# Performance work log

Hardware: AMD Instinct MI355X
Metric: run time of the kernel (lower is better)

Reference implementation:

```python
import jax, jax.numpy as jnp
import numpy as np

N = 100000   # nodes
F = 128      # input features
H = 128      # hidden = 2*output_dim
Z = 64       # output_dim
E = 1600000  # message-passing edges
EP = 200000  # pos/neg decode edges each


def setup_inputs() -> dict:
    key = jax.random.key(0)
    ks = jax.random.split(key, 6)
    x = jax.random.normal(ks[0], (N, F), dtype=jnp.float32)
    edge_index = jax.random.randint(ks[1], (2, E), 0, N, dtype=jnp.int64)
    pos_edge = jax.random.randint(ks[2], (2, EP), 0, N, dtype=jnp.int64)
    neg_edge = jax.random.randint(ks[3], (2, EP), 0, N, dtype=jnp.int64)
    W1 = jax.random.normal(ks[4], (F, H), dtype=jnp.float32) / np.float32(np.sqrt(F))
    b1 = jnp.zeros((H,), jnp.float32)
    W2 = jax.random.normal(ks[5], (H, Z), dtype=jnp.float32) / np.float32(np.sqrt(H))
    b2 = jnp.zeros((Z,), jnp.float32)
    return dict(x=x, W1=W1, b1=b1, W2=W2, b2=b2,
                edge_index=edge_index, pos_edge=pos_edge, neg_edge=neg_edge)


def _gcn_conv(x, src, dst, norm, W, b, n):
    # x' = scatter_add_dst(norm * (x @ W)[src]) + b   (GCNConv, sym-normalized, self-loops)
    h = x @ W                         # [N, out]
    msg = h[src] * norm[:, None]      # [E+N, out] gather + scale
    out = jax.ops.segment_sum(msg, dst, num_segments=n)
    return out + b


def reference(x, W1, b1, W2, b2, edge_index, pos_edge, neg_edge):
    # add self-loops (GCNConv default)
    loop = jnp.arange(N, dtype=edge_index.dtype)
    src = jnp.concatenate([edge_index[0], loop])
    dst = jnp.concatenate([edge_index[1], loop])
    # symmetric normalization deg^-1/2[src] * deg^-1/2[dst]
    deg = jax.ops.segment_sum(jnp.ones(dst.shape, x.dtype), dst, num_segments=N)
    dinv = jnp.where(deg > 0, jax.lax.rsqrt(deg), 0.0)
    norm = dinv[src] * dinv[dst]
    # encoder: GCN -> ReLU -> GCN
    h = jax.nn.relu(_gcn_conv(x, src, dst, norm, W1, b1, N))
    latent = _gcn_conv(h, src, dst, norm, W2, b2, N)
    # decoder: edge dot products on pos+neg edges
    e = jnp.concatenate([pos_edge, neg_edge], axis=-1)  # [2, 2*EP]
    logits = jnp.sum(latent[e[0]] * latent[e[1]], axis=-1)
    return logits
```

## Files before the change

### kernel.cpp

```cpp
#include <hip/hip_runtime.h>

#define N_NODES 100000
#define F_IN    128
#define H_DIM   128
#define Z_DIM   64
#define E_EDGES 1600000
#define EP_EDGES 200000

#define BSHIFT 7
#define NBUCK  ((N_NODES + 127) >> 7)
#define CHUNK  4096
#define NCHUNK ((E_EDGES + CHUNK - 1) / CHUNK)

typedef __attribute__((ext_vector_type(8))) short short8;
typedef __attribute__((ext_vector_type(4))) float f32x4;
typedef unsigned int uint;
typedef unsigned short ushort;

__device__ __forceinline__ ushort f2bf(float f) {
    uint u = __float_as_uint(f);
    u += 0x7fffu + ((u >> 16) & 1u);
    return (ushort)(u >> 16);
}
__device__ __forceinline__ float bflo(uint u) { return __uint_as_float(u << 16); }
__device__ __forceinline__ float bfhi(uint u) { return __uint_as_float(u & 0xffff0000u); }


__global__ __launch_bounds__(256) void wprep_kernel(const float* __restrict__ W1,
                                                    const float* __restrict__ W2,
                                                    ushort* __restrict__ W1T,
                                                    ushort* __restrict__ W2T,
                                                    int* __restrict__ gcur) {
    int i = blockIdx.x * 256 + threadIdx.x;
    if (i < 1024) gcur[i] = 0;
    if (i < 128 * 128) {
        int n = i >> 7, k = i & 127;
        W1T[i] = f2bf(W1[k * 128 + n]);
    }
    int j = i - 128 * 128;
    if (j >= 0 && j < 64 * 128) {
        int n = j >> 7, k = j & 127;
        W2T[j] = f2bf(W2[k * 64 + n]);
    }
}


__global__ __launch_bounds__(256) void bhist_kernel(const int* __restrict__ dst,
                                                    int* __restrict__ gcur,
                                                    int* __restrict__ tbl) {
    __shared__ int lh[NBUCK];
    for (int i = threadIdx.x; i < NBUCK; i += 256) lh[i] = 0;
    __syncthreads();
    int base = blockIdx.x * CHUNK;
    int end = min(base + CHUNK, E_EDGES);
    for (int e = base + threadIdx.x; e < end; e += 256)
        atomicAdd(&lh[dst[e] >> BSHIFT], 1);
    __syncthreads();
    int* trow = tbl + (size_t)blockIdx.x * NBUCK;
    for (int i = threadIdx.x; i < NBUCK; i += 256) {
        int c = lh[i];
        trow[i] = c;
        if (c) atomicAdd(&gcur[i], c);
    }
}


__global__ __launch_bounds__(1024) void bscan_kernel(int* __restrict__ gc) {
    __shared__ int s[1024];
    int t = threadIdx.x;
    int v = (t < NBUCK) ? gc[t] : 0;
    s[t] = v;
    __syncthreads();
    #pragma unroll
    for (int off = 1; off < 1024; off <<= 1) {
        int x = (t >= off) ? s[t - off] : 0;
        __syncthreads();
        s[t] += x;
        __syncthreads();
    }
    if (t < NBUCK) gc[t] = s[t] - v;
}


__global__ __launch_bounds__(512) void chunk_scan_kernel(int* __restrict__ tbl,
                                                         const int* __restrict__ gcur) {
    __shared__ int s[512];
    int b = blockIdx.x, t = threadIdx.x;
    int v = (t < NCHUNK) ? tbl[(size_t)t * NBUCK + b] : 0;
    s[t] = v;
    __syncthreads();
    #pragma unroll
    for (int off = 1; off < 512; off <<= 1) {
        int x = (t >= off) ? s[t - off] : 0;
        __syncthreads();
        s[t] += x;
        __syncthreads();
    }
    if (t < NCHUNK)
        tbl[(size_t)t * NBUCK + b] = gcur[b] + (s[t] - v);
}


__global__ __launch_bounds__(256) void bscatter_kernel(const int* __restrict__ src,
                                                       const int* __restrict__ dst,
                                                       const int* __restrict__ tbl,
                                                       int* __restrict__ sorted) {
    __shared__ int lbase[NBUCK];
    int c = blockIdx.x;
    const int* trow = tbl + (size_t)c * NBUCK;
    for (int i = threadIdx.x; i < NBUCK; i += 256) lbase[i] = trow[i];
    __syncthreads();
    int base = c * CHUNK;
    int end = min(base + CHUNK, E_EDGES);
    for (int e = base + threadIdx.x; e < end; e += 256) {
        int d = dst[e];
        int p = atomicAdd(&lbase[d >> BSHIFT], 1);
        sorted[p] = (src[e] << 7) | (d & 127);
    }
}


__global__ __launch_bounds__(256) void bucket_csr_kernel(const int* __restrict__ sorted,
                                                         const int* __restrict__ gcur,
                                                         int* __restrict__ csr,
                                                         int* __restrict__ ends,
                                                         float* __restrict__ dinv) {
    __shared__ int lcnt[4][128], lcur[4][128];
    int b = blockIdx.x, t = threadIdx.x;
    int wave = t >> 6;
    int bstart = gcur[b];
    int bend = (b + 1 < NBUCK) ? gcur[b + 1] : E_EDGES;
    if (t < 128) { lcnt[0][t] = 0; lcnt[1][t] = 0; }
    else { int u = t - 128; lcnt[2][u] = 0; lcnt[3][u] = 0; }
    __syncthreads();
    for (int i = bstart + t; i < bend; i += 256)
        atomicAdd(&lcnt[wave][sorted[i] & 127], 1);
    __syncthreads();
    if (t < 64) {
        int w0a = lcnt[0][t], w1a = lcnt[1][t], w2a = lcnt[2][t], w3a = lcnt[3][t];
        int w0b = lcnt[0][t + 64], w1b = lcnt[1][t + 64], w2b = lcnt[2][t + 64], w3b = lcnt[3][t + 64];
        int c0 = w0a + w1a + w2a + w3a;
        int c1 = w0b + w1b + w2b + w3b;
        int s0 = c0;
        #pragma unroll
        for (int d = 1; d < 64; d <<= 1) {
            int x = __shfl_up(s0, d, 64);
            if (t >= d) s0 += x;
        }
        int tot0 = __shfl(s0, 63, 64);
        int s1 = c1;
        #pragma unroll
        for (int d = 1; d < 64; d <<= 1) {
            int x = __shfl_up(s1, d, 64);
            if (t >= d) s1 += x;
        }
        s1 += tot0;
        int basea = bstart + s0 - c0;
        int baseb = bstart + s1 - c1;
        lcur[0][t] = basea;
        lcur[1][t] = basea + w0a;
        lcur[2][t] = basea + w0a + w1a;
        lcur[3][t] = basea + w0a + w1a + w2a;
        lcur[0][t + 64] = baseb;
        lcur[1][t + 64] = baseb + w0b;
        lcur[2][t + 64] = baseb + w0b + w1b;
        lcur[3][t + 64] = baseb + w0b + w1b + w2b;
        int n0 = b * 128 + t, n1 = n0 + 64;
        if (n0 < N_NODES) { ends[n0] = bstart + s0; dinv[n0] = rsqrtf(1.0f + (float)c0); }
        if (n1 < N_NODES) { ends[n1] = bstart + s1; dinv[n1] = rsqrtf(1.0f + (float)c1); }
    }
    __syncthreads();
    for (int i = bstart + t; i < bend; i += 256) {
        int v = sorted[i];
        int p = atomicAdd(&lcur[wave][v & 127], 1);
        csr[p] = v >> 7;
    }
}


template<int NC, bool A_F32>
__global__ __launch_bounds__(256) void gemm_mfma_kernel(const void* __restrict__ Ap,
                                                        const ushort* __restrict__ BT,
                                                        const float* __restrict__ dinv,
                                                        ushort* __restrict__ C, int M) {
    constexpr int NT = NC / 16;
    __shared__ ushort Bs[4 * NT * 64 * 8];

    for (int idx = threadIdx.x; idx < 4 * NT * 64; idx += 256) {
        int l   = idx & 63;
        int nt  = (idx >> 6) % NT;
        int kc  = idx / (64 * NT);
        int m16 = l & 15, quad = l >> 4;
        ((short8*)Bs)[idx] =
            *(const short8*)(BT + ((nt * 16 + m16) * 128 + kc * 32 + quad * 8));
    }
    __syncthreads();

    int wave = threadIdx.x >> 6, lane = threadIdx.x & 63;
    int m16 = lane & 15, quad = lane >> 4;
    int row0 = (blockIdx.x * 4 + wave) * 16;
    if (row0 >= M) return;
    int arow = row0 + m16;
    if (arow >= M) arow = M - 1;

    f32x4 acc[NT];
    #pragma unroll
    for (int t = 0; t < NT; ++t) acc[t] = (f32x4){0.f, 0.f, 0.f, 0.f};

    #pragma unroll
    for (int kc = 0; kc < 4; ++kc) {
        short8 a;
        if (A_F32) {
            const float* A = (const float*)Ap;
            const float4* p = (const float4*)(A + (size_t)arow * 128 + kc * 32 + quad * 8);
            float4 x0 = p[0], x1 = p[1];
            a[0] = (short)f2bf(x0.x); a[1] = (short)f2bf(x0.y);
            a[2] = (short)f2bf(x0.z); a[3] = (short)f2bf(x0.w);
            a[4] = (short)f2bf(x1.x); a[5] = (short)f2bf(x1.y);
            a[6] = (short)f2bf(x1.z); a[7] = (short)f2bf(x1.w);
        } else {
            a = *(const short8*)((const ushort*)Ap + (size_t)arow * 128 + kc * 32 + quad * 8);
        }
        #pragma unroll
        for (int nt = 0; nt < NT; ++nt) {
            short8 b = ((const short8*)Bs)[(kc * NT + nt) * 64 + lane];
            acc[nt] = __builtin_amdgcn_mfma_f32_16x16x32_bf16(a, b, acc[nt], 0, 0, 0);
        }
    }

    #pragma unroll
    for (int r = 0; r < 4; ++r) {
        int row = row0 + quad * 4 + r;
        if (row < M) {
            float dr = dinv[row];
            #pragma unroll
            for (int nt = 0; nt < NT; ++nt)
                C[(size_t)row * NC + nt * 16 + m16] = f2bf(acc[nt][r] * dr);
        }
    }
}


__global__ __launch_bounds__(256, 8) void gather128_kernel(const ushort* __restrict__ feat,
                                                           const float* __restrict__ bias,
                                                           const float* __restrict__ dinv,
                                                           const int* __restrict__ ends,
                                                           const int* __restrict__ csr,
                                                           ushort* __restrict__ out) {
    int wave = threadIdx.x >> 6, lane = threadIdx.x & 63;
    int q = lane >> 4, ql = lane & 15;
    int n = blockIdx.x * 4 + wave;
    const uint4* F = (const uint4*)feat;

    float a0 = 0.f, a1 = 0.f, a2 = 0.f, a3 = 0.f;
    float a4 = 0.f, a5 = 0.f, a6 = 0.f, a7 = 0.f;
    if (q == 0) {
        uint4 s = F[(uint)n * 16u + (uint)ql];
        a0 = bflo(s.x); a1 = bfhi(s.x); a2 = bflo(s.y); a3 = bfhi(s.y);
        a4 = bflo(s.z); a5 = bfhi(s.z); a6 = bflo(s.w); a7 = bfhi(s.w);
    }
    int j0 = n ? ends[n - 1] : 0, j1 = ends[n];
    for (int base = j0; base < j1; base += 64) {
        int m = min(64, j1 - base);
        int idxv = csr[base + min(lane, m - 1)];
        int nch = m >> 4;
        for (int c = 0; c < nch; ++c) {
            int e = c * 16 + q;
            int s0 = __shfl(idxv, e, 64);
            int s1 = __shfl(idxv, e + 4, 64);
            int s2 = __shfl(idxv, e + 8, 64);
            int s3 = __shfl(idxv, e + 12, 64);
            uint4 r0 = F[(uint)s0 * 16u + (uint)ql];
            uint4 r1 = F[(uint)s1 * 16u + (uint)ql];
            uint4 r2 = F[(uint)s2 * 16u + (uint)ql];
            uint4 r3 = F[(uint)s3 * 16u + (uint)ql];
            a0 += bflo(r0.x) + bflo(r1.x) + bflo(r2.x) + bflo(r3.x);
            a1 += bfhi(r0.x) + bfhi(r1.x) + bfhi(r2.x) + bfhi(r3.x);
            a2 += bflo(r0.y) + bflo(r1.y) + bflo(r2.y) + bflo(r3.y);
            a3 += bfhi(r0.y) + bfhi(r1.y) + bfhi(r2.y) + bfhi(r3.y);
            a4 += bflo(r0.z) + bflo(r1.z) + bflo(r2.z) + bflo(r3.z);
            a5 += bfhi(r0.z) + bfhi(r1.z) + bfhi(r2.z) + bfhi(r3.z);
            a6 += bflo(r0.w) + bflo(r1.w) + bflo(r2.w) + bflo(r3.w);
            a7 += bfhi(r0.w) + bfhi(r1.w) + bfhi(r2.w) + bfhi(r3.w);
        }
        if (nch * 16 < m) {
            int e = nch * 16 + q;
            int mc = m - 1;
            int t0 = __shfl(idxv, min(e,      mc), 64);
            int t1 = __shfl(idxv, min(e + 4,  mc), 64);
            int t2 = __shfl(idxv, min(e + 8,  mc), 64);
            int t3 = __shfl(idxv, min(e + 12, mc), 64);
            uint4 r0 = F[(uint)t0 * 16u + (uint)ql];
            uint4 r1 = F[(uint)t1 * 16u + (uint)ql];
            uint4 r2 = F[(uint)t2 * 16u + (uint)ql];
            uint4 r3 = F[(uint)t3 * 16u + (uint)ql];
            if (e < m) {
                a0 += bflo(r0.x); a1 += bfhi(r0.x); a2 += bflo(r0.y); a3 += bfhi(r0.y);
                a4 += bflo(r0.z); a5 += bfhi(r0.z); a6 += bflo(r0.w); a7 += bfhi(r0.w);
            }
            if (e + 4 < m) {
                a0 += bflo(r1.x); a1 += bfhi(r1.x); a2 += bflo(r1.y); a3 += bfhi(r1.y);
                a4 += bflo(r1.z); a5 += bfhi(r1.z); a6 += bflo(r1.w); a7 += bfhi(r1.w);
            }
            if (e + 8 < m) {
                a0 += bflo(r2.x); a1 += bfhi(r2.x); a2 += bflo(r2.y); a3 += bfhi(r2.y);
                a4 += bflo(r2.z); a5 += bfhi(r2.z); a6 += bflo(r2.w); a7 += bfhi(r2.w);
            }
            if (e + 12 < m) {
                a0 += bflo(r3.x); a1 += bfhi(r3.x); a2 += bflo(r3.y); a3 += bfhi(r3.y);
                a4 += bflo(r3.z); a5 += bfhi(r3.z); a6 += bflo(r3.w); a7 += bfhi(r3.w);
            }
        }
    }
    a0 += __shfl_xor(a0, 16, 64); a0 += __shfl_xor(a0, 32, 64);
    a1 += __shfl_xor(a1, 16, 64); a1 += __shfl_xor(a1, 32, 64);
    a2 += __shfl_xor(a2, 16, 64); a2 += __shfl_xor(a2, 32, 64);
    a3 += __shfl_xor(a3, 16, 64); a3 += __shfl_xor(a3, 32, 64);
    a4 += __shfl_xor(a4, 16, 64); a4 += __shfl_xor(a4, 32, 64);
    a5 += __shfl_xor(a5, 16, 64); a5 += __shfl_xor(a5, 32, 64);
    a6 += __shfl_xor(a6, 16, 64); a6 += __shfl_xor(a6, 32, 64);
    a7 += __shfl_xor(a7, 16, 64); a7 += __shfl_xor(a7, 32, 64);
    if (q == 0) {
        float dn = dinv[n];
        const float4* bp = (const float4*)(bias + ql * 8);
        float4 b0 = bp[0], b1v = bp[1];
        float r0 = fmaxf(b0.x + dn * a0, 0.f);
        float r1 = fmaxf(b0.y + dn * a1, 0.f);
        float r2 = fmaxf(b0.z + dn * a2, 0.f);
        float r3 = fmaxf(b0.w + dn * a3, 0.f);
        float r4 = fmaxf(b1v.x + dn * a4, 0.f);
        float r5 = fmaxf(b1v.y + dn * a5, 0.f);
        float r6 = fmaxf(b1v.z + dn * a6, 0.f);
        float r7 = fmaxf(b1v.w + dn * a7, 0.f);
        uint4 o;
        o.x = (uint)f2bf(r0) | ((uint)f2bf(r1) << 16);
        o.y = (uint)f2bf(r2) | ((uint)f2bf(r3) << 16);
        o.z = (uint)f2bf(r4) | ((uint)f2bf(r5) << 16);
        o.w = (uint)f2bf(r6) | ((uint)f2bf(r7) << 16);
        ((uint4*)out)[(uint)n * 16u + (uint)ql] = o;
    }
}


__global__ __launch_bounds__(256, 8) void gather64_kernel(const ushort* __restrict__ feat,
                                                          const float* __restrict__ bias,
                                                          const float* __restrict__ dinv,
                                                          const int* __restrict__ ends,
                                                          const int* __restrict__ csr,
                                                          ushort* __restrict__ outB) {
    int wave = threadIdx.x >> 6, lane = threadIdx.x & 63;
    int g = lane >> 5, c = lane & 31;
    int n = blockIdx.x * 4 + wave;
    const uint* F = (const uint*)feat;

    float a0 = 0.f, a1 = 0.f;
    uint su = F[(uint)n * 32u + (uint)c];
    if (g == 0) { a0 = bflo(su); a1 = bfhi(su); }

    int j0 = n ? ends[n - 1] : 0, j1 = ends[n];
    j0 = __builtin_amdgcn_readfirstlane(j0);
    j1 = __builtin_amdgcn_readfirstlane(j1);

    for (int base = j0; base < j1; base += 64) {
        int m = min(64, j1 - base);
        int idxv = __builtin_nontemporal_load(csr + base + min(lane, m - 1));
        int e = 0;
        for (; e + 8 <= m; e += 8) {
            int sa0 = __builtin_amdgcn_readlane(idxv, e + 0);
            int sb0 = __builtin_amdgcn_readlane(idxv, e + 1);
            int sa1 = __builtin_amdgcn_readlane(idxv, e + 2);
            int sb1 = __builtin_amdgcn_readlane(idxv, e + 3);
            int sa2 = __builtin_amdgcn_readlane(idxv, e + 4);
            int sb2 = __builtin_amdgcn_readlane(idxv, e + 5);
            int sa3 = __builtin_amdgcn_readlane(idxv, e + 6);
            int sb3 = __builtin_amdgcn_readlane(idxv, e + 7);
            uint p0 = (uint)(g ? sb0 : sa0);
            uint p1 = (uint)(g ? sb1 : sa1);
            uint p2 = (uint)(g ? sb2 : sa2);
            uint p3 = (uint)(g ? sb3 : sa3);
            uint r0 = F[p0 * 32u + (uint)c];
            uint r1 = F[p1 * 32u + (uint)c];
            uint r2 = F[p2 * 32u + (uint)c];
            uint r3 = F[p3 * 32u + (uint)c];
            a0 += bflo(r0) + bflo(r1);
            a1 += bfhi(r0) + bfhi(r1);
            a0 += bflo(r2) + bflo(r3);
            a1 += bfhi(r2) + bfhi(r3);
        }
        for (; e + 2 <= m; e += 2) {
            int sa = __builtin_amdgcn_readlane(idxv, e);
            int sb = __builtin_amdgcn_readlane(idxv, e + 1);
            uint p = (uint)(g ? sb : sa);
            uint r = F[p * 32u + (uint)c];
            a0 += bflo(r); a1 += bfhi(r);
        }
        if (e < m) {
            int s = __builtin_amdgcn_readlane(idxv, e);
            uint r = F[(uint)s * 32u + (uint)c];
            if (g == 0) { a0 += bflo(r); a1 += bfhi(r); }
        }
    }
    a0 += __shfl_xor(a0, 32, 64);
    a1 += __shfl_xor(a1, 32, 64);
    if (g == 0) {
        float dn = dinv[n];
        float2 bv = ((const float2*)bias)[c];
        float o0 = bv.x + dn * a0;
        float o1 = bv.y + dn * a1;
        ((uint*)outB)[(uint)n * 32u + (uint)c] = (uint)f2bf(o0) | ((uint)f2bf(o1) << 16);
    }
}


__global__ __launch_bounds__(256) void decode_kernel(const ushort* __restrict__ latentB,
                                                     const int* __restrict__ pos,
                                                     const int* __restrict__ neg,
                                                     float* __restrict__ out) {
    int gwave = (blockIdx.x * 256 + threadIdx.x) >> 6;
    int lane = threadIdx.x & 63;
    int half = lane >> 5, sl = lane & 31;
    const uint* L = (const uint*)latentB;
    int e0 = gwave * 8 + half * 4;
    if (e0 >= 2 * EP_EDGES) return;

    int ia[4], ib[4];
    #pragma unroll
    for (int u = 0; u < 4; ++u) {
        int edge = e0 + u;
        if (edge < EP_EDGES) {
            ia[u] = pos[edge];
            ib[u] = pos[EP_EDGES + edge];
        } else {
            int e2 = edge - EP_EDGES;
            ia[u] = neg[e2];
            ib[u] = neg[EP_EDGES + e2];
        }
    }
    uint la[4], lb[4];
    #pragma unroll
    for (int u = 0; u < 4; ++u) {
        la[u] = L[(size_t)ia[u] * 32 + sl];
        lb[u] = L[(size_t)ib[u] * 32 + sl];
    }
    float v[4];
    #pragma unroll
    for (int u = 0; u < 4; ++u)
        v[u] = bflo(la[u]) * bflo(lb[u]) + bfhi(la[u]) * bfhi(lb[u]);
    #pragma unroll
    for (int u = 0; u < 4; ++u) {
        float s = v[u];
        #pragma unroll
        for (int off = 16; off > 0; off >>= 1) s += __shfl_down(s, off, 64);
        if (sl == 0) out[e0 + u] = s;
    }
}


extern "C" void kernel_launch(void* const* d_in, const int* in_sizes, int n_in,
                              void* d_out, int out_size, void* d_ws, size_t ws_size,
                              hipStream_t stream) {
    const float* x  = (const float*)d_in[0];
    const float* W1 = (const float*)d_in[1];
    const float* b1 = (const float*)d_in[2];
    const float* W2 = (const float*)d_in[3];
    const float* b2 = (const float*)d_in[4];
    const int* edge_index = (const int*)d_in[5];
    const int* pos = (const int*)d_in[6];
    const int* neg = (const int*)d_in[7];
    float* out = (float*)d_out;

    const int* src = edge_index;
    const int* dst = edge_index + E_EDGES;

    float*  dinv   = (float*)d_ws;
    int*    ends   = (int*)(dinv + N_NODES);
    int*    gcur   = ends + N_NODES;
    int*    tbl    = gcur + 1024;
    int*    sorted = tbl + NCHUNK * NBUCK;
    int*    csr    = sorted + E_EDGES;
    ushort* W1T    = (ushort*)(csr + E_EDGES);
    ushort* W2T    = W1T + 128 * 128;
    ushort* bufH   = (ushort*)(((uintptr_t)(W2T + 64 * 128) + 255) & ~(uintptr_t)255);
    ushort* bufR   = bufH + (size_t)N_NODES * 128;

    wprep_kernel<<<96, 256, 0, stream>>>(W1, W2, W1T, W2T, gcur);

    bhist_kernel<<<NCHUNK, 256, 0, stream>>>(dst, gcur, tbl);
    bscan_kernel<<<1, 1024, 0, stream>>>(gcur);
    chunk_scan_kernel<<<NBUCK, 512, 0, stream>>>(tbl, gcur);
    bscatter_kernel<<<NCHUNK, 256, 0, stream>>>(src, dst, tbl, sorted);
    bucket_csr_kernel<<<NBUCK, 256, 0, stream>>>(sorted, gcur, csr, ends, dinv);

    const int GEMM_GRID = (N_NODES + 63) / 64;

    gemm_mfma_kernel<128, true><<<GEMM_GRID, 256, 0, stream>>>(x, W1T, dinv, bufH, N_NODES);

    gather128_kernel<<<N_NODES / 4, 256, 0, stream>>>(bufH, b1, dinv, ends, csr, bufR);

    gemm_mfma_kernel<64, false><<<GEMM_GRID, 256, 0, stream>>>(bufR, W2T, dinv, bufH, N_NODES);

    ushort* latentB = bufR;
    gather64_kernel<<<N_NODES / 4, 256, 0, stream>>>(bufH, b2, dinv, ends, csr, latentB);

    decode_kernel<<<(2 * EP_EDGES) / 32, 256, 0, stream>>>(latentB, pos, neg, out);
}
```

Before: 312.4 us.

## Replace two-level bucket sort CSR build with direct atomic counting sort

Swaps the bucketed two-pass CSR construction (chunk histograms, per-chunk scans, bucket scatter, in-bucket sort) for a plain per-node degree histogram with global atomics, a three-kernel prefix scan, and a direct atomic scatter into CSR. This drops the intermediate sorted buffer and the large chunk×bucket table, plus one full pass over the edges. In exchange it uses 1.6M global atomics on random addresses twice, and the within-node edge order becomes nondeterministic. That order changes floating-point summation order, and the random placement may hurt gather locality.

```diff
diff --git a/kernel.cpp b/kernel.cpp
--- a/kernel.cpp
+++ b/kernel.cpp
@@ -7,10 +7,8 @@
 #define E_EDGES 1600000
 #define EP_EDGES 200000
 
-#define BSHIFT 7
-#define NBUCK  ((N_NODES + 127) >> 7)
-#define CHUNK  4096
-#define NCHUNK ((E_EDGES + CHUNK - 1) / CHUNK)
+#define PSB  1024
+#define NPB  ((N_NODES + PSB - 1) / PSB)
 
 typedef __attribute__((ext_vector_type(8))) short short8;
 typedef __attribute__((ext_vector_type(4))) float f32x4;
@@ -30,9 +28,9 @@
                                                     const float* __restrict__ W2,
                                                     ushort* __restrict__ W1T,
                                                     ushort* __restrict__ W2T,
-                                                    int* __restrict__ gcur) {
+                                                    int* __restrict__ deg) {
     int i = blockIdx.x * 256 + threadIdx.x;
-    if (i < 1024) gcur[i] = 0;
+    if (i < N_NODES) deg[i] = 0;
     if (i < 128 * 128) {
         int n = i >> 7, k = i & 127;
         W1T[i] = f2bf(W1[k * 128 + n]);
@@ -45,135 +43,80 @@
 }
 
 
-__global__ __launch_bounds__(256) void bhist_kernel(const int* __restrict__ dst,
-                                                    int* __restrict__ gcur,
-                                                    int* __restrict__ tbl) {
-    __shared__ int lh[NBUCK];
-    for (int i = threadIdx.x; i < NBUCK; i += 256) lh[i] = 0;
+__global__ __launch_bounds__(256) void deghist_kernel(const int* __restrict__ dst,
+                                                      int* __restrict__ deg) {
+    int e = blockIdx.x * 256 + threadIdx.x;
+    if (e < E_EDGES) atomicAdd(&deg[dst[e]], 1);
+}
+
+__global__ __launch_bounds__(PSB) void pscan1_kernel(const int* __restrict__ deg,
+                                                     int* __restrict__ bsum) {
+    int i = blockIdx.x * PSB + threadIdx.x;
+    int v = (i < N_NODES) ? deg[i] : 0;
+    #pragma unroll
+    for (int off = 32; off > 0; off >>= 1) v += __shfl_down(v, off, 64);
+    __shared__ int ws_[16];
+    int wv = threadIdx.x >> 6, ln = threadIdx.x & 63;
+    if (ln == 0) ws_[wv] = v;
     __syncthreads();
-    int base = blockIdx.x * CHUNK;
-    int end = min(base + CHUNK, E_EDGES);
-    for (int e = base + threadIdx.x; e < end; e += 256)
-        atomicAdd(&lh[dst[e] >> BSHIFT], 1);
-    __syncthreads();
-    int* trow = tbl + (size_t)blockIdx.x * NBUCK;
-    for (int i = threadIdx.x; i < NBUCK; i += 256) {
-        int c = lh[i];
-        trow[i] = c;
-        if (c) atomicAdd(&gcur[i], c);
-    }
-}
-
-
-__global__ __launch_bounds__(1024) void bscan_kernel(int* __restrict__ gc) {
-    __shared__ int s[1024];
+    if (threadIdx.x < 16) {
+        int x = ws_[threadIdx.x];
+        #pragma unroll
+        for (int off = 8; off > 0; off >>= 1) x += __shfl_down(x, off, 16);
+        if (threadIdx.x == 0) bsum[blockIdx.x] = x;
+    }
+}
+
+__global__ __launch_bounds__(128) void pscan2_kernel(int* __restrict__ bsum) {
+    __shared__ int s[128];
     int t = threadIdx.x;
-    int v = (t < NBUCK) ? gc[t] : 0;
+    int v = (t < NPB) ? bsum[t] : 0;
     s[t] = v;
     __syncthreads();
     #pragma unroll
-    for (int off = 1; off < 1024; off <<= 1) {
+    for (int off = 1; off < 128; off <<= 1) {
         int x = (t >= off) ? s[t - off] : 0;
         __syncthreads();
         s[t] += x;
         __syncthreads();
     }
-    if (t < NBUCK) gc[t] = s[t] - v;
-}
-
-
-__global__ __launch_bounds__(512) void chunk_scan_kernel(int* __restrict__ tbl,
-                                                         const int* __restrict__ gcur) {
-    __shared__ int s[512];
-    int b = blockIdx.x, t = threadIdx.x;
-    int v = (t < NCHUNK) ? tbl[(size_t)t * NBUCK + b] : 0;
+    if (t < NPB) bsum[t] = s[t] - v;
+}
+
+__global__ __launch_bounds__(PSB) void pscan3_kernel(const int* __restrict__ deg,
+                                                     const int* __restrict__ bsum,
+                                                     int* __restrict__ ends,
+                                                     int* __restrict__ cur,
+                                                     float* __restrict__ dinv) {
+    __shared__ int s[PSB];
+    int t = threadIdx.x;
+    int i = blockIdx.x * PSB + t;
+    int v = (i < N_NODES) ? deg[i] : 0;
     s[t] = v;
     __syncthreads();
     #pragma unroll
-    for (int off = 1; off < 512; off <<= 1) {
+    for (int off = 1; off < PSB; off <<= 1) {
         int x = (t >= off) ? s[t - off] : 0;
         __syncthreads();
         s[t] += x;
         __syncthreads();
     }
-    if (t < NCHUNK)
-        tbl[(size_t)t * NBUCK + b] = gcur[b] + (s[t] - v);
-}
-
-
-__global__ __launch_bounds__(256) void bscatter_kernel(const int* __restrict__ src,
-                                                       const int* __restrict__ dst,
-                                                       const int* __restrict__ tbl,
-                                                       int* __restrict__ sorted) {
-    __shared__ int lbase[NBUCK];
-    int c = blockIdx.x;
-    const int* trow = tbl + (size_t)c * NBUCK;
-    for (int i = threadIdx.x; i < NBUCK; i += 256) lbase[i] = trow[i];
-    __syncthreads();
-    int base = c * CHUNK;
-    int end = min(base + CHUNK, E_EDGES);
-    for (int e = base + threadIdx.x; e < end; e += 256) {
-        int d = dst[e];
-        int p = atomicAdd(&lbase[d >> BSHIFT], 1);
-        sorted[p] = (src[e] << 7) | (d & 127);
-    }
-}
-
-
-__global__ __launch_bounds__(256) void bucket_csr_kernel(const int* __restrict__ sorted,
-                                                         const int* __restrict__ gcur,
-                                                         int* __restrict__ csr,
-                                                         int* __restrict__ ends,
-                                                         float* __restrict__ dinv) {
-    __shared__ int lcnt[4][128], lcur[4][128];
-    int b = blockIdx.x, t = threadIdx.x;
-    int wave = t >> 6;
-    int bstart = gcur[b];
-    int bend = (b + 1 < NBUCK) ? gcur[b + 1] : E_EDGES;
-    if (t < 128) { lcnt[0][t] = 0; lcnt[1][t] = 0; }
-    else { int u = t - 128; lcnt[2][u] = 0; lcnt[3][u] = 0; }
-    __syncthreads();
-    for (int i = bstart + t; i < bend; i += 256)
-        atomicAdd(&lcnt[wave][sorted[i] & 127], 1);
-    __syncthreads();
-    if (t < 64) {
-        int w0a = lcnt[0][t], w1a = lcnt[1][t], w2a = lcnt[2][t], w3a = lcnt[3][t];
-        int w0b = lcnt[0][t + 64], w1b = lcnt[1][t + 64], w2b = lcnt[2][t + 64], w3b = lcnt[3][t + 64];
-        int c0 = w0a + w1a + w2a + w3a;
-        int c1 = w0b + w1b + w2b + w3b;
-        int s0 = c0;
-        #pragma unroll
-        for (int d = 1; d < 64; d <<= 1) {
-            int x = __shfl_up(s0, d, 64);
-            if (t >= d) s0 += x;
-        }
-        int tot0 = __shfl(s0, 63, 64);
-        int s1 = c1;
-        #pragma unroll
-        for (int d = 1; d < 64; d <<= 1) {
-            int x = __shfl_up(s1, d, 64);
-            if (t >= d) s1 += x;
-        }
-        s1 += tot0;
-        int basea = bstart + s0 - c0;
-        int baseb = bstart + s1 - c1;
-        lcur[0][t] = basea;
-        lcur[1][t] = basea + w0a;
-        lcur[2][t] = basea + w0a + w1a;
-        lcur[3][t] = basea + w0a + w1a + w2a;
-        lcur[0][t + 64] = baseb;
-        lcur[1][t + 64] = baseb + w0b;
-        lcur[2][t + 64] = baseb + w0b + w1b;
-        lcur[3][t + 64] = baseb + w0b + w1b + w2b;
-        int n0 = b * 128 + t, n1 = n0 + 64;
-        if (n0 < N_NODES) { ends[n0] = bstart + s0; dinv[n0] = rsqrtf(1.0f + (float)c0); }
-        if (n1 < N_NODES) { ends[n1] = bstart + s1; dinv[n1] = rsqrtf(1.0f + (float)c1); }
-    }
-    __syncthreads();
-    for (int i = bstart + t; i < bend; i += 256) {
-        int v = sorted[i];
-        int p = atomicAdd(&lcur[wave][v & 127], 1);
-        csr[p] = v >> 7;
+    if (i < N_NODES) {
+        int start = bsum[blockIdx.x] + s[t] - v;
+        cur[i] = start;
+        ends[i] = start + v;
+        dinv[i] = rsqrtf(1.0f + (float)v);
+    }
+}
+
+__global__ __launch_bounds__(256) void scatter_kernel(const int* __restrict__ src,
+                                                      const int* __restrict__ dst,
+                                                      int* __restrict__ cur,
+                                                      int* __restrict__ csr) {
+    int e = blockIdx.x * 256 + threadIdx.x;
+    if (e < E_EDGES) {
+        int p = atomicAdd(&cur[dst[e]], 1);
+        csr[p] = src[e];
     }
 }
 
@@ -474,22 +417,22 @@
 
     float*  dinv   = (float*)d_ws;
     int*    ends   = (int*)(dinv + N_NODES);
-    int*    gcur   = ends + N_NODES;
-    int*    tbl    = gcur + 1024;
-    int*    sorted = tbl + NCHUNK * NBUCK;
-    int*    csr    = sorted + E_EDGES;
+    int*    deg    = ends + N_NODES;
+    int*    cur    = deg + N_NODES;
+    int*    bsum   = cur + N_NODES;
+    int*    csr    = bsum + 128;
     ushort* W1T    = (ushort*)(csr + E_EDGES);
     ushort* W2T    = W1T + 128 * 128;
     ushort* bufH   = (ushort*)(((uintptr_t)(W2T + 64 * 128) + 255) & ~(uintptr_t)255);
     ushort* bufR   = bufH + (size_t)N_NODES * 128;
 
-    wprep_kernel<<<96, 256, 0, stream>>>(W1, W2, W1T, W2T, gcur);
-
-    bhist_kernel<<<NCHUNK, 256, 0, stream>>>(dst, gcur, tbl);
-    bscan_kernel<<<1, 1024, 0, stream>>>(gcur);
-    chunk_scan_kernel<<<NBUCK, 512, 0, stream>>>(tbl, gcur);
-    bscatter_kernel<<<NCHUNK, 256, 0, stream>>>(src, dst, tbl, sorted);
-    bucket_csr_kernel<<<NBUCK, 256, 0, stream>>>(sorted, gcur, csr, ends, dinv);
+    wprep_kernel<<<(N_NODES + 255) / 256, 256, 0, stream>>>(W1, W2, W1T, W2T, deg);
+
+    deghist_kernel<<<(E_EDGES + 255) / 256, 256, 0, stream>>>(dst, deg);
+    pscan1_kernel<<<NPB, PSB, 0, stream>>>(deg, bsum);
+    pscan2_kernel<<<1, 128, 0, stream>>>(bsum);
+    pscan3_kernel<<<NPB, PSB, 0, stream>>>(deg, bsum, ends, cur, dinv);
+    scatter_kernel<<<(E_EDGES + 255) / 256, 256, 0, stream>>>(src, dst, cur, csr);
 
     const int GEMM_GRID = (N_NODES + 63) / 64;
 
```

Result: slower. 451.6 us (+44.6%).
